# Kernel optimization log

Hardware: AMD Instinct MI355X
Metric: run time of the kernel (lower is better)

## Reference

```python
import jax, jax.numpy as jnp
import numpy as np

T = 64      # num_time_steps
N = 2048    # nodes
D = 512     # input_dim == hid_dim == out_dim (required by code's residual/split structure)
WEIGHT = 0.5  # residual blend weight from __init__
NEG_BIG = -2.0**32 + 1.0


def setup_inputs() -> dict:
    key = jax.random.key(0)
    ks = jax.random.split(key, 7)
    s = 1.0 / np.sqrt(D)
    return {
        "inputs": jax.random.normal(ks[0], (T, N, D), dtype=jnp.float32),  # stacked snapshots [T,N,F]
        "pos_emb": jax.random.normal(ks[1], (T, D), dtype=jnp.float32) * s,
        "Wq": jax.random.normal(ks[2], (D, D), dtype=jnp.float32) * s,
        "Wk": jax.random.normal(ks[3], (D, D), dtype=jnp.float32) * s,
        "Wv": jax.random.normal(ks[4], (D, D), dtype=jnp.float32) * s,
        "lin_w": jax.random.normal(ks[5], (D, D), dtype=jnp.float32) * s,  # nn.Linear weight [out,in]
        "lin_b": jax.random.normal(ks[6], (D,), dtype=jnp.float32) * 0.01,
    }


def reference(inputs, pos_emb, Wq, Wk, Wv, lin_w, lin_b):
    # stack + permute(1,0,2): [T,N,D] -> [N,T,D]
    x = jnp.transpose(inputs, (1, 0, 2))
    # position embedding gathered by arange(T), broadcast over nodes
    temporal = x + pos_emb[None, :, :]                      # [N,T,D]
    q = jnp.einsum('ntd,de->nte', temporal, Wq)             # [N,T,D]
    k = jnp.einsum('ntd,de->nte', temporal, Wk)
    v = jnp.einsum('ntd,de->nte', temporal, Wv)
    scores = jnp.einsum('nqd,nkd->nqk', q, k)               # [N,T,T] (no sqrt(d) scaling, as in source)
    causal = jnp.tril(jnp.ones((T, T), dtype=bool))
    scores = jnp.where(causal[None], scores, jnp.float32(NEG_BIG))
    attn = jax.nn.softmax(scores, axis=2)                   # dropout inactive (eval mode)
    out = jnp.einsum('nqk,nkd->nqd', attn, v)               # [N,T,D]
    # n_heads == 1: split along dim0 + concat along dim2 is the identity
    ff = jax.nn.relu(jnp.einsum('ntd,ed->nte', out, lin_w) + lin_b) + out
    return WEIGHT * ff + temporal                           # residual=True
```

## Files before the change

### kernel.cpp

```cpp
#include <hip/hip_runtime.h>


#define TT 64
#define NN 2048
#define DD 512

typedef _Float16 f16x8 __attribute__((ext_vector_type(8)));
typedef float    f32x4 __attribute__((ext_vector_type(4)));

#define MFMA16(a,b,c) __builtin_amdgcn_mfma_f32_16x16x32_f16((a),(b),(c),0,0,0)

__global__ __launch_bounds__(256) void prep_weights(
    const float* __restrict__ Wq, const float* __restrict__ Wk,
    const float* __restrict__ Wv, const float* __restrict__ lw,
    _Float16* __restrict__ out)
{
  int gid = blockIdx.x * 256 + threadIdx.x;
  int mat = gid >> 15;
  int r   = gid & 32767;
  int tile = r >> 6;
  int l    = r & 63;
  int rowblk = tile >> 4;
  int kbb    = tile & 15;
  int e  = rowblk * 16 + (l & 15);
  int d0 = kbb * 32 + (l >> 4) * 8;
  union { _Float16 h[8]; uint4 u; } o;
  if (mat < 3) {
    const float* W = (mat == 0) ? Wq : (mat == 1) ? Wk : Wv;
    #pragma unroll
    for (int j = 0; j < 8; ++j)
      o.h[j] = (_Float16)W[(size_t)(d0 + j) * DD + e];
  } else {
    #pragma unroll
    for (int j = 0; j < 8; ++j)
      o.h[j] = (_Float16)lw[(size_t)e * DD + d0 + j];
  }
  *(uint4*)(out + (size_t)gid * 8) = o.u;
}

__global__ __launch_bounds__(512) void attn_fused(
    const float* __restrict__ x, const float* __restrict__ pos,
    const _Float16* __restrict__ WF, _Float16* __restrict__ outp)
{
  __shared__ char smem[109568];
  char* const tstp = smem;
  char* const qdp  = smem + 65536;
  char* const scb  = smem + 65536;
  char* const vdp  = smem + 65536;
  char* const kdp  = smem + 82944;
  char* const atn  = smem + 100352;

  const int n    = blockIdx.x;
  const int tid  = threadIdx.x;
  const int wid  = tid >> 6;
  const int lane = tid & 63;
  const int quad = lane >> 4;
  const int l15  = lane & 15;
  const size_t scrbase = (size_t)n * 65536 + 32768;

  const _Float16* const Fq = WF;
  const _Float16* const Fk = WF + 262144;
  const _Float16* const Fv = WF + 524288;

  {
    const int row = tid >> 3, si = tid & 7;
    const float* xr = x + ((size_t)row * NN + n) * DD;
    const float* pr = pos + (size_t)row * DD;
    char* const dst = tstp + row * 1024;
    const int swz = (row & 7) << 4;
    #pragma unroll
    for (int kb = 0; kb < 16; ++kb) {
      f32x4 xv = *(const f32x4*)(xr + kb * 32 + 4 * si);
      f32x4 pv = *(const f32x4*)(pr + kb * 32 + 4 * si);
      union { _Float16 h[4]; unsigned long long u; } o;
      #pragma unroll
      for (int j = 0; j < 4; ++j) o.h[j] = (_Float16)(xv[j] + pv[j]);
      *(unsigned long long*)(dst + ((kb * 64 + si * 8) ^ swz)) = o.u;
    }
  }
  __syncthreads();

  const int rswz = (l15 & 7) << 4;
  f32x4 sacc[2] = {};

  for (int ph = 0; ph < 2; ++ph) {
    f32x4 acc[4][4] = {};
    const bool isK = (wid >= 4);
    const int  esl = wid & 3;
    const _Float16* const fwave =
        (isK ? Fk : Fq) + (size_t)(ph * 16 + esl * 4) * 8192 + (size_t)lane * 8;

    #pragma unroll
    for (int kb = 0; kb < 16; ++kb) {
      f16x8 bf[4];
      #pragma unroll
      for (int ct = 0; ct < 4; ++ct)
        bf[ct] = *(const f16x8*)(fwave + (size_t)kb * 512 + (size_t)ct * 8192);
      f16x8 af[4];
      #pragma unroll
      for (int rt = 0; rt < 4; ++rt)
        af[rt] = *(const f16x8*)(tstp + (16 * rt + l15) * 1024 +
                                 ((kb * 64 + quad * 16) ^ rswz));
      #pragma unroll
      for (int ct = 0; ct < 4; ++ct)
        #pragma unroll
        for (int rt = 0; rt < 4; ++rt)
          acc[rt][ct] = MFMA16(af[rt], bf[ct], acc[rt][ct]);
    }

    for (int r = 0; r < 2; ++r) {
      __syncthreads();
      if ((esl >> 1) == r) {
        char* dst = isK ? kdp : qdp;
        const int colbase = (esl & 1) * 64;
        #pragma unroll
        for (int rt = 0; rt < 4; ++rt)
          #pragma unroll
          for (int ct = 0; ct < 4; ++ct)
            #pragma unroll
            for (int rg = 0; rg < 4; ++rg)
              *(_Float16*)(dst + (16*rt + quad*4 + rg)*272 + (colbase + 16*ct + l15)*2)
                  = (_Float16)acc[rt][ct][rg];
      }
      __syncthreads();
      const int srt = wid >> 1, sct0 = (wid & 1) * 2;
      #pragma unroll
      for (int ks = 0; ks < 4; ++ks) {
        f16x8 aq = *(const f16x8*)(qdp + (16*srt + l15)*272 + ks*64 + quad*16);
        #pragma unroll
        for (int j = 0; j < 2; ++j) {
          f16x8 bk = *(const f16x8*)(kdp + (16*(sct0+j) + l15)*272 + ks*64 + quad*16);
          sacc[j] = MFMA16(aq, bk, sacc[j]);
        }
      }
    }
  }

  __syncthreads();
  {
    const int srt = wid >> 1, sct0 = (wid & 1) * 2;
    #pragma unroll
    for (int j = 0; j < 2; ++j)
      #pragma unroll
      for (int rg = 0; rg < 4; ++rg)
        *(float*)(scb + (16*srt + quad*4 + rg)*272 + (16*(sct0+j) + l15)*4) = sacc[j][rg];
  }
  __syncthreads();
  {
    const int row = tid >> 3, i = tid & 7;
    f32x4 s0 = *(const f32x4*)(scb + row*272 + 32*i);
    f32x4 s1 = *(const f32x4*)(scb + row*272 + 32*i + 16);
    float s[8] = { s0[0],s0[1],s0[2],s0[3], s1[0],s1[1],s1[2],s1[3] };
    float m = -3.0e38f;
    #pragma unroll
    for (int j = 0; j < 8; ++j) if (8*i + j <= row) m = fmaxf(m, s[j]);
    m = fmaxf(m, __shfl_xor(m, 1));
    m = fmaxf(m, __shfl_xor(m, 2));
    m = fmaxf(m, __shfl_xor(m, 4));
    float e[8]; float sum = 0.f;
    #pragma unroll
    for (int j = 0; j < 8; ++j) {
      e[j] = (8*i + j <= row) ? __expf(s[j] - m) : 0.f;
      sum += e[j];
    }
    sum += __shfl_xor(sum, 1);
    sum += __shfl_xor(sum, 2);
    sum += __shfl_xor(sum, 4);
    const float inv = 1.0f / sum;
    union { _Float16 h[8]; uint4 u; } o;
    #pragma unroll
    for (int j = 0; j < 8; ++j) o.h[j] = (_Float16)(e[j] * inv);
    *(uint4*)(atn + row*144 + 16*i) = o.u;
  }

  f32x4 vacc[4][4] = {};
  {
    const _Float16* const fwv = Fv + (size_t)(wid * 4) * 8192 + (size_t)lane * 8;
    #pragma unroll
    for (int kb = 0; kb < 16; ++kb) {
      f16x8 bf[4];
      #pragma unroll
      for (int ct = 0; ct < 4; ++ct)
        bf[ct] = *(const f16x8*)(fwv + (size_t)kb * 512 + (size_t)ct * 8192);
      f16x8 af[4];
      #pragma unroll
      for (int rt = 0; rt < 4; ++rt)
        af[rt] = *(const f16x8*)(tstp + (16 * rt + l15) * 1024 +
                                 ((kb * 64 + quad * 16) ^ rswz));
      #pragma unroll
      for (int ct = 0; ct < 4; ++ct)
        #pragma unroll
        for (int rt = 0; rt < 4; ++rt)
          vacc[rt][ct] = MFMA16(af[rt], bf[ct], vacc[rt][ct]);
    }
  }

  __syncthreads();
  char* const vd = vdp + wid * 4352;
  #pragma unroll
  for (int h = 0; h < 2; ++h) {
    #pragma unroll
    for (int c = 0; c < 2; ++c) {
      const int ct = 2*h + c;
      #pragma unroll
      for (int rt = 0; rt < 4; ++rt)
        #pragma unroll
        for (int rg = 0; rg < 4; ++rg)
          *(_Float16*)(vd + (16*c + l15)*136 + (16*rt + quad*4 + rg)*2)
              = (_Float16)vacc[rt][ct][rg];
    }
    f32x4 oacc[2][4] = {};
    #pragma unroll
    for (int ks = 0; ks < 2; ++ks) {
      f16x8 av[2];
      #pragma unroll
      for (int mt = 0; mt < 2; ++mt)
        av[mt] = *(const f16x8*)(vd + (16*mt + l15)*136 + ks*64 + quad*16);
      #pragma unroll
      for (int nt = 0; nt < 4; ++nt) {
        f16x8 ba = *(const f16x8*)(atn + (16*nt + l15)*144 + ks*64 + quad*16);
        #pragma unroll
        for (int mt = 0; mt < 2; ++mt)
          oacc[mt][nt] = MFMA16(av[mt], ba, oacc[mt][nt]);
      }
    }
    #pragma unroll
    for (int mt = 0; mt < 2; ++mt)
      #pragma unroll
      for (int nt = 0; nt < 4; ++nt) {
        const int d0 = 64*wid + 32*h + 16*mt + quad*4;
        const int tq = 16*nt + l15;
        union { _Float16 h4[4]; uint2 u; } o;
        #pragma unroll
        for (int rg = 0; rg < 4; ++rg) o.h4[rg] = (_Float16)oacc[mt][nt][rg];
        *(uint2*)(outp + scrbase + (size_t)tq * DD + d0) = o.u;
      }
  }
}

__global__ __launch_bounds__(512) void ff_final(
    const _Float16* __restrict__ outp, const float* __restrict__ x,
    const float* __restrict__ pos, const _Float16* __restrict__ lwF,
    const float* __restrict__ lb, float* __restrict__ y)
{
  __shared__ char smem[65536];

  const int n = blockIdx.x;
  const int tid = threadIdx.x;
  const int wid = tid >> 6, lane = tid & 63, quad = lane >> 4, l15 = lane & 15;
  const size_t scrbase = (size_t)n * 65536 + 32768;

  {
    const int row = tid >> 3, si = tid & 7;
    const _Float16* sr = outp + scrbase + (size_t)row * DD;
    char* const dst = smem + row * 1024;
    const int swz = (row & 7) << 4;
    #pragma unroll
    for (int kb = 0; kb < 16; ++kb)
      *(unsigned long long*)(dst + ((kb * 64 + si * 8) ^ swz)) =
          *(const unsigned long long*)(sr + kb * 32 + 4 * si);
  }
  __syncthreads();

  const int rswz = (l15 & 7) << 4;
  const _Float16* const fA = lwF + (size_t)(wid * 4) * 8192 + (size_t)lane * 8;

  f32x4 acc[4][4] = {};
  #pragma unroll
  for (int kb = 0; kb < 16; ++kb) {
    f16x8 af[4];
    #pragma unroll
    for (int mt = 0; mt < 4; ++mt)
      af[mt] = *(const f16x8*)(fA + (size_t)kb * 512 + (size_t)mt * 8192);
    #pragma unroll
    for (int nt = 0; nt < 4; ++nt) {
      f16x8 bo = *(const f16x8*)(smem + (16 * nt + l15) * 1024 +
                                 ((kb * 64 + quad * 16) ^ rswz));
      #pragma unroll
      for (int mt = 0; mt < 4; ++mt)
        acc[mt][nt] = MFMA16(af[mt], bo, acc[mt][nt]);
    }
  }

  #pragma unroll
  for (int mt = 0; mt < 4; ++mt) {
    const int e0 = wid*64 + 16*mt + quad*4;
    f32x4 bias = *(const f32x4*)(lb + e0);
    #pragma unroll
    for (int nt = 0; nt < 4; ++nt) {
      const int tq = 16*nt + l15;
      const size_t base = ((size_t)n * TT + tq) * DD + e0;
      union { _Float16 h4[4]; unsigned long long u; } ov;
      ov.u = *(const unsigned long long*)(smem + tq * 1024 + ((2 * e0) ^ rswz));
      f32x4 xv = *(const f32x4*)(x + ((size_t)tq * NN + n) * DD + e0);
      f32x4 pv = *(const f32x4*)(pos + (size_t)tq * DD + e0);
      f32x4 ro;
      #pragma unroll
      for (int rg = 0; rg < 4; ++rg) {
        float ff = acc[mt][nt][rg] + bias[rg];
        ff = ff > 0.f ? ff : 0.f;
        ro[rg] = 0.5f * (ff + (float)ov.h4[rg]) + xv[rg] + pv[rg];
      }
      *(f32x4*)(y + base) = ro;
    }
  }
}

extern "C" void kernel_launch(void* const* d_in, const int* in_sizes, int n_in,
                              void* d_out, int out_size, void* d_ws, size_t ws_size,
                              hipStream_t stream) {
  (void)in_sizes; (void)n_in; (void)out_size; (void)ws_size;
  const float* x   = (const float*)d_in[0];
  const float* pos = (const float*)d_in[1];
  const float* Wq  = (const float*)d_in[2];
  const float* Wk  = (const float*)d_in[3];
  const float* Wv  = (const float*)d_in[4];
  const float* lw  = (const float*)d_in[5];
  const float* lb  = (const float*)d_in[6];
  _Float16* wsW = (_Float16*)d_ws;

  prep_weights<<<512, 256, 0, stream>>>(Wq, Wk, Wv, lw, wsW);
  attn_fused<<<2048, 512, 0, stream>>>(x, pos, wsW, (_Float16*)d_out);
  ff_final<<<2048, 512, 0, stream>>>((const _Float16*)d_out, x, pos,
                                     wsW + 786432, lb, (float*)d_out);
}
```

Measured before the change: 953.5 us.

## Software-pipeline projection GEMM loads with register multi-buffering and raw barriers

Rewrites the Q/K/V projection loops and the feed-forward GEMM loop as explicitly software-pipelined sequences. Weight fragments are prefetched from global memory several k-steps ahead and LDS A-fragments two steps ahead, using rotating register buffers. __syncthreads is replaced by a raw barrier that waits only on LDS counters and adds a scheduling fence, and occupancy hints are added to launch_bounds (2 blocks for attn_fused, 4 for ff_final). The aim is to hide global and LDS latency behind MFMA work, at the cost of more registers, which may clash with the occupancy hints and cause spills.

New measurement: 962.8 us. About the same (+1.0%).

```diff
diff --git a/kernel.cpp b/kernel.cpp
--- a/kernel.cpp
+++ b/kernel.cpp
@@ -9,6 +9,59 @@
 typedef float    f32x4 __attribute__((ext_vector_type(4)));
 
 #define MFMA16(a,b,c) __builtin_amdgcn_mfma_f32_16x16x32_f16((a),(b),(c),0,0,0)
+
+#define RAW_BARRIER() do { \
+    asm volatile("s_waitcnt lgkmcnt(0)" ::: "memory"); \
+    __builtin_amdgcn_s_barrier(); \
+    __builtin_amdgcn_sched_barrier(0); \
+  } while (0)
+
+#define LDW4(W, F, KB) do { \
+    W[0] = *(const f16x8*)((F) + (size_t)(KB) * 512); \
+    W[1] = *(const f16x8*)((F) + (size_t)(KB) * 512 + 8192); \
+    W[2] = *(const f16x8*)((F) + (size_t)(KB) * 512 + 16384); \
+    W[3] = *(const f16x8*)((F) + (size_t)(KB) * 512 + 24576); \
+  } while (0)
+
+#define LDA4(A, BASE, KB) do { \
+    A[0] = *(const f16x8*)((BASE) + (l15) * 1024 + ((((KB) * 64) + quad * 16) ^ rswz)); \
+    A[1] = *(const f16x8*)((BASE) + (16 + l15) * 1024 + ((((KB) * 64) + quad * 16) ^ rswz)); \
+    A[2] = *(const f16x8*)((BASE) + (32 + l15) * 1024 + ((((KB) * 64) + quad * 16) ^ rswz)); \
+    A[3] = *(const f16x8*)((BASE) + (48 + l15) * 1024 + ((((KB) * 64) + quad * 16) ^ rswz)); \
+  } while (0)
+
+#define PRJ_STEP(WC, AC, ACC, F, BASE, KB) do { \
+    _Pragma("unroll") \
+    for (int rt_ = 0; rt_ < 4; ++rt_) { \
+      _Pragma("unroll") \
+      for (int ct_ = 0; ct_ < 4; ++ct_) \
+        ACC[rt_][ct_] = MFMA16(AC[rt_], WC[ct_], ACC[rt_][ct_]); \
+    } \
+    if ((KB) + 3 < 16) LDW4(WC, F, (KB) + 3); \
+    if ((KB) + 2 < 16) LDA4(AC, BASE, (KB) + 2); \
+  } while (0)
+
+#define PROJ16(F, BASE, ACC) do { \
+    f16x8 wA_[4], wB_[4], wC_[4], aA_[4], aB_[4]; \
+    LDW4(wA_, F, 0); LDW4(wB_, F, 1); LDW4(wC_, F, 2); \
+    LDA4(aA_, BASE, 0); LDA4(aB_, BASE, 1); \
+    PRJ_STEP(wA_, aA_, ACC, F, BASE, 0); \
+    PRJ_STEP(wB_, aB_, ACC, F, BASE, 1); \
+    PRJ_STEP(wC_, aA_, ACC, F, BASE, 2); \
+    PRJ_STEP(wA_, aB_, ACC, F, BASE, 3); \
+    PRJ_STEP(wB_, aA_, ACC, F, BASE, 4); \
+    PRJ_STEP(wC_, aB_, ACC, F, BASE, 5); \
+    PRJ_STEP(wA_, aA_, ACC, F, BASE, 6); \
+    PRJ_STEP(wB_, aB_, ACC, F, BASE, 7); \
+    PRJ_STEP(wC_, aA_, ACC, F, BASE, 8); \
+    PRJ_STEP(wA_, aB_, ACC, F, BASE, 9); \
+    PRJ_STEP(wB_, aA_, ACC, F, BASE, 10); \
+    PRJ_STEP(wC_, aB_, ACC, F, BASE, 11); \
+    PRJ_STEP(wA_, aA_, ACC, F, BASE, 12); \
+    PRJ_STEP(wB_, aB_, ACC, F, BASE, 13); \
+    PRJ_STEP(wC_, aA_, ACC, F, BASE, 14); \
+    PRJ_STEP(wA_, aB_, ACC, F, BASE, 15); \
+  } while (0)
 
 __global__ __launch_bounds__(256) void prep_weights(
     const float* __restrict__ Wq, const float* __restrict__ Wk,
@@ -38,7 +91,7 @@
   *(uint4*)(out + (size_t)gid * 8) = o.u;
 }
 
-__global__ __launch_bounds__(512) void attn_fused(
+__global__ __launch_bounds__(512, 2) void attn_fused(
     const float* __restrict__ x, const float* __restrict__ pos,
     const _Float16* __restrict__ WF, _Float16* __restrict__ outp)
 {
@@ -78,7 +131,7 @@
       *(unsigned long long*)(dst + ((kb * 64 + si * 8) ^ swz)) = o.u;
     }
   }
-  __syncthreads();
+  RAW_BARRIER();
 
   const int rswz = (l15 & 7) << 4;
   f32x4 sacc[2] = {};
@@ -90,26 +143,10 @@
     const _Float16* const fwave =
         (isK ? Fk : Fq) + (size_t)(ph * 16 + esl * 4) * 8192 + (size_t)lane * 8;
 
-    #pragma unroll
-    for (int kb = 0; kb < 16; ++kb) {
-      f16x8 bf[4];
-      #pragma unroll
-      for (int ct = 0; ct < 4; ++ct)
-        bf[ct] = *(const f16x8*)(fwave + (size_t)kb * 512 + (size_t)ct * 8192);
-      f16x8 af[4];
-      #pragma unroll
-      for (int rt = 0; rt < 4; ++rt)
-        af[rt] = *(const f16x8*)(tstp + (16 * rt + l15) * 1024 +
-                                 ((kb * 64 + quad * 16) ^ rswz));
-      #pragma unroll
-      for (int ct = 0; ct < 4; ++ct)
-        #pragma unroll
-        for (int rt = 0; rt < 4; ++rt)
-          acc[rt][ct] = MFMA16(af[rt], bf[ct], acc[rt][ct]);
-    }
+    PROJ16(fwave, tstp, acc);
 
     for (int r = 0; r < 2; ++r) {
-      __syncthreads();
+      RAW_BARRIER();
       if ((esl >> 1) == r) {
         char* dst = isK ? kdp : qdp;
         const int colbase = (esl & 1) * 64;
@@ -122,7 +159,7 @@
               *(_Float16*)(dst + (16*rt + quad*4 + rg)*272 + (colbase + 16*ct + l15)*2)
                   = (_Float16)acc[rt][ct][rg];
       }
-      __syncthreads();
+      RAW_BARRIER();
       const int srt = wid >> 1, sct0 = (wid & 1) * 2;
       #pragma unroll
       for (int ks = 0; ks < 4; ++ks) {
@@ -136,7 +173,7 @@
     }
   }
 
-  __syncthreads();
+  RAW_BARRIER();
   {
     const int srt = wid >> 1, sct0 = (wid & 1) * 2;
     #pragma unroll
@@ -145,7 +182,7 @@
       for (int rg = 0; rg < 4; ++rg)
         *(float*)(scb + (16*srt + quad*4 + rg)*272 + (16*(sct0+j) + l15)*4) = sacc[j][rg];
   }
-  __syncthreads();
+  RAW_BARRIER();
   {
     const int row = tid >> 3, i = tid & 7;
     f32x4 s0 = *(const f32x4*)(scb + row*272 + 32*i);
@@ -176,26 +213,10 @@
   f32x4 vacc[4][4] = {};
   {
     const _Float16* const fwv = Fv + (size_t)(wid * 4) * 8192 + (size_t)lane * 8;
-    #pragma unroll
-    for (int kb = 0; kb < 16; ++kb) {
-      f16x8 bf[4];
-      #pragma unroll
-      for (int ct = 0; ct < 4; ++ct)
-        bf[ct] = *(const f16x8*)(fwv + (size_t)kb * 512 + (size_t)ct * 8192);
-      f16x8 af[4];
-      #pragma unroll
-      for (int rt = 0; rt < 4; ++rt)
-        af[rt] = *(const f16x8*)(tstp + (16 * rt + l15) * 1024 +
-                                 ((kb * 64 + quad * 16) ^ rswz));
-      #pragma unroll
-      for (int ct = 0; ct < 4; ++ct)
-        #pragma unroll
-        for (int rt = 0; rt < 4; ++rt)
-          vacc[rt][ct] = MFMA16(af[rt], bf[ct], vacc[rt][ct]);
-    }
-  }
-
-  __syncthreads();
+    PROJ16(fwv, tstp, vacc);
+  }
+
+  RAW_BARRIER();
   char* const vd = vdp + wid * 4352;
   #pragma unroll
   for (int h = 0; h < 2; ++h) {
@@ -238,7 +259,7 @@
   }
 }
 
-__global__ __launch_bounds__(512) void ff_final(
+__global__ __launch_bounds__(512, 4) void ff_final(
     const _Float16* __restrict__ outp, const float* __restrict__ x,
     const float* __restrict__ pos, const _Float16* __restrict__ lwF,
     const float* __restrict__ lb, float* __restrict__ y)
@@ -260,27 +281,38 @@
       *(unsigned long long*)(dst + ((kb * 64 + si * 8) ^ swz)) =
           *(const unsigned long long*)(sr + kb * 32 + 4 * si);
   }
-  __syncthreads();
 
   const int rswz = (l15 & 7) << 4;
   const _Float16* const fA = lwF + (size_t)(wid * 4) * 8192 + (size_t)lane * 8;
 
+  f16x8 wA_[4], wB_[4];
+  LDW4(wA_, fA, 0); LDW4(wB_, fA, 1);
+  RAW_BARRIER();
+
   f32x4 acc[4][4] = {};
-  #pragma unroll
-  for (int kb = 0; kb < 16; ++kb) {
-    f16x8 af[4];
-    #pragma unroll
-    for (int mt = 0; mt < 4; ++mt)
-      af[mt] = *(const f16x8*)(fA + (size_t)kb * 512 + (size_t)mt * 8192);
-    #pragma unroll
-    for (int nt = 0; nt < 4; ++nt) {
-      f16x8 bo = *(const f16x8*)(smem + (16 * nt + l15) * 1024 +
-                                 ((kb * 64 + quad * 16) ^ rswz));
-      #pragma unroll
-      for (int mt = 0; mt < 4; ++mt)
-        acc[mt][nt] = MFMA16(af[mt], bo, acc[mt][nt]);
-    }
-  }
+  #define FF_STEP(WC, KB) do { \
+      f16x8 bo0 = *(const f16x8*)(smem + (l15) * 1024 + ((((KB) * 64) + quad * 16) ^ rswz)); \
+      f16x8 bo1 = *(const f16x8*)(smem + (16 + l15) * 1024 + ((((KB) * 64) + quad * 16) ^ rswz)); \
+      f16x8 bo2 = *(const f16x8*)(smem + (32 + l15) * 1024 + ((((KB) * 64) + quad * 16) ^ rswz)); \
+      f16x8 bo3 = *(const f16x8*)(smem + (48 + l15) * 1024 + ((((KB) * 64) + quad * 16) ^ rswz)); \
+      _Pragma("unroll") \
+      for (int mt_ = 0; mt_ < 4; ++mt_) { \
+        acc[mt_][0] = MFMA16(WC[mt_], bo0, acc[mt_][0]); \
+        acc[mt_][1] = MFMA16(WC[mt_], bo1, acc[mt_][1]); \
+        acc[mt_][2] = MFMA16(WC[mt_], bo2, acc[mt_][2]); \
+        acc[mt_][3] = MFMA16(WC[mt_], bo3, acc[mt_][3]); \
+      } \
+      if ((KB) + 2 < 16) LDW4(WC, fA, (KB) + 2); \
+    } while (0)
+  FF_STEP(wA_, 0);  FF_STEP(wB_, 1);
+  FF_STEP(wA_, 2);  FF_STEP(wB_, 3);
+  FF_STEP(wA_, 4);  FF_STEP(wB_, 5);
+  FF_STEP(wA_, 6);  FF_STEP(wB_, 7);
+  FF_STEP(wA_, 8);  FF_STEP(wB_, 9);
+  FF_STEP(wA_, 10); FF_STEP(wB_, 11);
+  FF_STEP(wA_, 12); FF_STEP(wB_, 13);
+  FF_STEP(wA_, 14); FF_STEP(wB_, 15);
+  #undef FF_STEP
 
   #pragma unroll
   for (int mt = 0; mt < 4; ++mt) {
```
